# Performance work log

Hardware: AMD Instinct MI355X
Metric: run time of the kernel (lower is better)

The kernel has to match this reference:

```python
import jax, jax.numpy as jnp
import numpy as np

B, C = 8388608, 4
OTHERS_IDX = 3

def setup_inputs() -> dict:
    key = jax.random.key(0)
    k1, k2 = jax.random.split(key)
    preds = jax.random.normal(k1, (B, C), dtype=jnp.float32)
    target = jax.random.randint(k2, (B,), 0, C, dtype=jnp.int64)
    return {"preds": preds, "target": target, "others_idx": OTHERS_IDX}

def reference(preds, target, others_idx):
    # softmax over class dim (dim=1 in the torch module)
    probs = jax.nn.softmax(preds, axis=1)              # [B, C]
    p_o = probs[:, others_idx]                          # [B]
    s = probs.sum(axis=1)                               # [B] (== 1, but computed as in original)
    # per-sample false-negative error (samples whose target IS the 'others' class)
    fne_i = 0.5 * ((s - p_o) ** 2 + (p_o - 1.0) ** 2)   # [B]
    # per-sample false-positive error (samples whose target is NOT 'others')
    fpe_i = 0.5 * ((-p_o) ** 2 + p_o ** 2)              # [B]
    is_others = (target == others_idx)                  # [B] bool
    fne_num = jnp.sum(is_others).astype(probs.dtype)
    fpe_num = jnp.sum(~is_others).astype(probs.dtype)
    fne = jnp.sum(jnp.where(is_others, fne_i, 0.0)) / fne_num
    fpe = jnp.sum(jnp.where(is_others, 0.0, fpe_i)) / fpe_num
    return fpe + fne
```

## Files before the change

kernel.cpp:

```cpp
#include <hip/hip_runtime.h>


#define BLOCK 256
#define ROWS 8

__device__ __forceinline__ void mfe_row(float4 x, int t, int o,
                                        float& fne_acc, float& fpe_acc,
                                        float& cnt_acc) {
    float m = fmaxf(fmaxf(x.x, x.y), fmaxf(x.z, x.w));
    float e0 = __expf(x.x - m);
    float e1 = __expf(x.y - m);
    float e2 = __expf(x.z - m);
    float e3 = __expf(x.w - m);
    float S = (e0 + e1) + (e2 + e3);
    float r = 1.0f / S;
    float p0 = e0 * r, p1 = e1 * r, p2 = e2 * r, p3 = e3 * r;
    float s = ((p0 + p1) + p2) + p3;
    float po = (o == 0) ? p0 : (o == 1) ? p1 : (o == 2) ? p2 : p3;

    float d1 = s - po;
    float d2 = po - 1.0f;
    float fne_i = 0.5f * (d1 * d1 + d2 * d2);
    float fpe_i = po * po;

    bool is_o = (t == o);
    fne_acc += is_o ? fne_i : 0.0f;
    fpe_acc += is_o ? 0.0f : fpe_i;
    cnt_acc += is_o ? 1.0f : 0.0f;
}

__global__ __launch_bounds__(BLOCK) void mfe_partial(
    const float4* __restrict__ preds,
    const int* __restrict__ target,
    const int* __restrict__ others_idx_p,
    float* __restrict__ fne_part,
    float* __restrict__ fpe_part,
    float* __restrict__ cnt_part,
    int n_rows)
{
    const int o = *others_idx_p;
    int tid = blockIdx.x * blockDim.x + threadIdx.x;
    int nth = gridDim.x * blockDim.x;

    float fne_acc = 0.0f, fpe_acc = 0.0f, cnt_acc = 0.0f;

    if (tid + (ROWS - 1) * nth < n_rows) {
        float4 x[ROWS];
        int    t[ROWS];
        #pragma unroll
        for (int k = 0; k < ROWS; ++k) {
            x[k] = preds[tid + k * nth];
            t[k] = target[tid + k * nth];
        }
        __builtin_amdgcn_sched_barrier(0);
        #pragma unroll
        for (int k = 0; k < ROWS; ++k)
            mfe_row(x[k], t[k], o, fne_acc, fpe_acc, cnt_acc);
    } else {
        for (int i = tid; i < n_rows; i += nth)
            mfe_row(preds[i], target[i], o, fne_acc, fpe_acc, cnt_acc);
    }

    #pragma unroll
    for (int off = 32; off > 0; off >>= 1) {
        fne_acc += __shfl_down(fne_acc, off, 64);
        fpe_acc += __shfl_down(fpe_acc, off, 64);
        cnt_acc += __shfl_down(cnt_acc, off, 64);
    }

    if ((threadIdx.x & 63) == 0) {
        int part = blockIdx.x * (BLOCK / 64) + (threadIdx.x >> 6);
        fne_part[part] = fne_acc;
        fpe_part[part] = fpe_acc;
        cnt_part[part] = cnt_acc;
    }
}

__global__ __launch_bounds__(1024) void mfe_final(
    const float* __restrict__ fne_part,
    const float* __restrict__ fpe_part,
    const float* __restrict__ cnt_part,
    int nparts, int n_rows, float* __restrict__ out)
{
    double fn = 0.0, fp = 0.0, c = 0.0;
    for (int i = threadIdx.x; i < nparts; i += blockDim.x) {
        fn += (double)fne_part[i];
        fp += (double)fpe_part[i];
        c  += (double)cnt_part[i];
    }
    #pragma unroll
    for (int off = 32; off > 0; off >>= 1) {
        fn += __shfl_down(fn, off, 64);
        fp += __shfl_down(fp, off, 64);
        c  += __shfl_down(c, off, 64);
    }
    __shared__ double s_fn[16], s_fp[16], s_c[16];
    int wave = threadIdx.x >> 6;
    int lane = threadIdx.x & 63;
    if (lane == 0) { s_fn[wave] = fn; s_fp[wave] = fp; s_c[wave] = c; }
    __syncthreads();

    if (threadIdx.x == 0) {
        double tfn = 0.0, tfp = 0.0, tc = 0.0;
        int nwaves = blockDim.x >> 6;
        for (int w = 0; w < nwaves; ++w) { tfn += s_fn[w]; tfp += s_fp[w]; tc += s_c[w]; }
        double fne_num = tc;
        double fpe_num = (double)n_rows - fne_num;
        double res = 0.0;
        if (fpe_num > 0.0) res += tfp / fpe_num;
        if (fne_num > 0.0) res += tfn / fne_num;
        out[0] = (float)res;
    }
}

extern "C" void kernel_launch(void* const* d_in, const int* in_sizes, int n_in,
                              void* d_out, int out_size, void* d_ws, size_t ws_size,
                              hipStream_t stream) {
    const float4* preds = (const float4*)d_in[0];
    const int* target = (const int*)d_in[1];
    const int* others_idx = (const int*)d_in[2];
    float* out = (float*)d_out;

    int n_rows = in_sizes[0] / 4;

    int grid = (n_rows + BLOCK * ROWS - 1) / (BLOCK * ROWS);
    int nparts = grid * (BLOCK / 64);

    float* fne_part = (float*)d_ws;
    float* fpe_part = fne_part + nparts;
    float* cnt_part = fpe_part + nparts;

    mfe_partial<<<grid, BLOCK, 0, stream>>>(preds, target, others_idx,
                                            fne_part, fpe_part, cnt_part, n_rows);
    mfe_final<<<1, 1024, 0, stream>>>(fne_part, fpe_part, cnt_part,
                                      nparts, n_rows, out);
}
```

Baseline: 222.4 us.

## Stage preds and targets through LDS with direct global-to-LDS loads

Replaces the direct per-thread register loads with global_load_lds transfers that stage 2048-row tiles of predictions and targets into shared memory. Each 1024-thread block then walks 8 tiles, with a fixed grid of 512 blocks. The aim is wider, more coalesced loads and less register pressure. In exchange it adds two block barriers per tile with no double buffering, and it drops the tail handling by hardcoding the grid to exactly cover 8M rows.

Result: no change. 218.5 us (-1.8%).

```diff
diff --git a/kernel.cpp b/kernel.cpp
--- a/kernel.cpp
+++ b/kernel.cpp
@@ -1,10 +1,21 @@
 #include <hip/hip_runtime.h>
 
 
-#define BLOCK 256
-#define ROWS 8
+#define BLOCK 1024
+#define TILE 2048
+#define NTILES 8
+#define GRID 512
 
-__device__ __forceinline__ void mfe_row(float4 x, int t, int o,
+typedef float vfloat4 __attribute__((ext_vector_type(4)));
+typedef int   vint4   __attribute__((ext_vector_type(4)));
+
+__device__ __forceinline__ void gl_lds16(const void* g, void* l) {
+    __builtin_amdgcn_global_load_lds(
+        (const __attribute__((address_space(1))) void*)g,
+        (__attribute__((address_space(3))) void*)l, 16, 0, 0);
+}
+
+__device__ __forceinline__ void mfe_row(vfloat4 x, int t, int o,
                                         float& fne_acc, float& fpe_acc,
                                         float& cnt_acc) {
     float m = fmaxf(fmaxf(x.x, x.y), fmaxf(x.z, x.w));
@@ -30,7 +41,7 @@
 }
 
 __global__ __launch_bounds__(BLOCK) void mfe_partial(
-    const float4* __restrict__ preds,
+    const vfloat4* __restrict__ preds,
     const int* __restrict__ target,
     const int* __restrict__ others_idx_p,
     float* __restrict__ fne_part,
@@ -38,27 +49,40 @@
     float* __restrict__ cnt_part,
     int n_rows)
 {
+    __shared__ vfloat4 xs[TILE];
+    __shared__ int     ts[TILE];
+
     const int o = *others_idx_p;
-    int tid = blockIdx.x * blockDim.x + threadIdx.x;
-    int nth = gridDim.x * blockDim.x;
+    const int tid  = threadIdx.x;
+    const int wave = tid >> 6;
+    const int lane = tid & 63;
+    const int block_row0 = blockIdx.x * (TILE * NTILES);
 
     float fne_acc = 0.0f, fpe_acc = 0.0f, cnt_acc = 0.0f;
 
-    if (tid + (ROWS - 1) * nth < n_rows) {
-        float4 x[ROWS];
-        int    t[ROWS];
-        #pragma unroll
-        for (int k = 0; k < ROWS; ++k) {
-            x[k] = preds[tid + k * nth];
-            t[k] = target[tid + k * nth];
+    for (int t = 0; t < NTILES; ++t) {
+        const int row0 = block_row0 + t * TILE;
+
+        {
+            int seg = wave * 2;
+            gl_lds16(preds + row0 + seg * 64 + lane, &xs[seg * 64]);
+            gl_lds16(preds + row0 + (seg + 1) * 64 + lane, &xs[(seg + 1) * 64]);
+            if (wave < 8) {
+                const vint4* gt = (const vint4*)(target + row0) + wave * 64 + lane;
+                gl_lds16(gt, (int*)ts + wave * 256);
+            }
         }
-        __builtin_amdgcn_sched_barrier(0);
-        #pragma unroll
-        for (int k = 0; k < ROWS; ++k)
-            mfe_row(x[k], t[k], o, fne_acc, fpe_acc, cnt_acc);
-    } else {
-        for (int i = tid; i < n_rows; i += nth)
-            mfe_row(preds[i], target[i], o, fne_acc, fpe_acc, cnt_acc);
+        __syncthreads();
+
+        {
+            vfloat4 x0 = xs[tid];
+            vfloat4 x1 = xs[tid + 1024];
+            int t0 = ts[tid];
+            int t1 = ts[tid + 1024];
+            mfe_row(x0, t0, o, fne_acc, fpe_acc, cnt_acc);
+            mfe_row(x1, t1, o, fne_acc, fpe_acc, cnt_acc);
+        }
+        __syncthreads();
     }
 
     #pragma unroll
@@ -68,8 +92,8 @@
         cnt_acc += __shfl_down(cnt_acc, off, 64);
     }
 
-    if ((threadIdx.x & 63) == 0) {
-        int part = blockIdx.x * (BLOCK / 64) + (threadIdx.x >> 6);
+    if (lane == 0) {
+        int part = blockIdx.x * (BLOCK / 64) + wave;
         fne_part[part] = fne_acc;
         fpe_part[part] = fpe_acc;
         cnt_part[part] = cnt_acc;
@@ -116,21 +140,20 @@
 extern "C" void kernel_launch(void* const* d_in, const int* in_sizes, int n_in,
                               void* d_out, int out_size, void* d_ws, size_t ws_size,
                               hipStream_t stream) {
-    const float4* preds = (const float4*)d_in[0];
+    const vfloat4* preds = (const vfloat4*)d_in[0];
     const int* target = (const int*)d_in[1];
     const int* others_idx = (const int*)d_in[2];
     float* out = (float*)d_out;
 
     int n_rows = in_sizes[0] / 4;
 
-    int grid = (n_rows + BLOCK * ROWS - 1) / (BLOCK * ROWS);
-    int nparts = grid * (BLOCK / 64);
+    int nparts = GRID * (BLOCK / 64);
 
     float* fne_part = (float*)d_ws;
     float* fpe_part = fne_part + nparts;
     float* cnt_part = fpe_part + nparts;
 
-    mfe_partial<<<grid, BLOCK, 0, stream>>>(preds, target, others_idx,
+    mfe_partial<<<GRID, BLOCK, 0, stream>>>(preds, target, others_idx,
                                             fne_part, fpe_part, cnt_part, n_rows);
     mfe_final<<<1, 1024, 0, stream>>>(fne_part, fpe_part, cnt_part,
                                       nparts, n_rows, out);
```
